# Performance work log

Hardware: AMD Instinct MI355X
Metric: run time of the kernel (lower is better)

The kernel has to match this reference:

```python
import jax, jax.numpy as jnp
import numpy as np

B, N, H, G, WIN, MH = 8, 8192, 128, 16, 3, 16
EPS = 1e-8


def _edges(n, w):
    # local sequence edges: i -> j for j in [i-w, i+w], j != i, 0 <= j < n
    i = np.arange(n)
    off = np.concatenate([np.arange(-w, 0), np.arange(1, w + 1)])
    j = i[:, None] + off[None, :]
    m = (j >= 0) & (j < n)
    src = np.broadcast_to(i[:, None], j.shape)[m]
    dst = j[m]
    return jnp.asarray(src, jnp.int32), jnp.asarray(dst, jnp.int32)


def setup_inputs() -> dict:
    key = jax.random.key(0)
    ks = jax.random.split(key, 10)
    d = {}
    d['x_scalar'] = jax.random.normal(ks[0], (B, N, H), jnp.float32)
    d['vec'] = jax.random.normal(ks[1], (B, N, 3, H), jnp.float32)
    d['W_geom'] = jax.random.normal(ks[2], (H, G), jnp.float32) / np.sqrt(H).astype(np.float32)
    d['q_w1'] = jax.random.normal(ks[3], (2, MH), jnp.float32) * 0.5
    d['q_b1'] = jnp.zeros((MH,), jnp.float32)
    d['q_w2'] = jax.random.normal(ks[4], (MH, 1), jnp.float32) * 0.25
    d['q_b2'] = jnp.zeros((1,), jnp.float32)
    d['k_w1'] = jax.random.normal(ks[5], (2, MH), jnp.float32) * 0.5
    d['k_b1'] = jnp.zeros((MH,), jnp.float32)
    d['k_w2'] = jax.random.normal(ks[6], (MH, 1), jnp.float32) * 0.25
    d['k_b2'] = jnp.zeros((1,), jnp.float32)
    d['Wq'] = jax.random.normal(ks[7], (G, H), jnp.float32) / np.sqrt(G).astype(np.float32)
    d['bq'] = jnp.zeros((H,), jnp.float32)
    d['Wk'] = jax.random.normal(ks[8], (G, H), jnp.float32) / np.sqrt(G).astype(np.float32)
    d['bk'] = jnp.zeros((H,), jnp.float32)
    return d


def _mlp(f, w1, b1, w2, b2):
    # f: (B,E,G,2) -> (B,E,G)
    return (jax.nn.silu(f @ w1 + b1) @ w2 + b2)[..., 0]


def reference(x_scalar, vec, W_geom, q_w1, q_b1, q_w2, q_b2,
              k_w1, k_b1, k_w2, k_b2, Wq, bq, Wk, bk):
    b, n, h = x_scalar.shape
    src, dst = _edges(n, WIN)
    # project vectors into geometry subspace: (B,N,3,G)
    vec_geom = jnp.einsum('bnch,hg->bncg', vec, W_geom)
    v_i = vec_geom[:, src]          # (B,E,3,G)
    v_j = vec_geom[:, dst]
    b_ij = v_j - v_i
    norm_b = jnp.maximum(jnp.linalg.norm(b_ij, axis=2, keepdims=True), EPS)
    e_ij = b_ij / norm_b            # unit edge directions (B,E,3,G)
    # scatter-add edge directions back to source nodes: (B,N,3,G)
    u = jnp.zeros((b, n, 3, G), x_scalar.dtype).at[:, src].add(e_ij)
    u_i = u[:, src]
    u_j = u[:, dst]
    dot_ui_e = (u_i * e_ij).sum(axis=2)                       # (B,E,G)
    norm_ui = jnp.maximum(jnp.linalg.norm(u_i, axis=2), EPS)
    ang_ij = jnp.clip(dot_ui_e / norm_ui, -1.0, 1.0)
    u_i_perp = u_i - dot_ui_e[:, :, None, :] * e_ij
    dot_uj_e = (u_j * e_ij).sum(axis=2)
    u_j_perp = u_j - dot_uj_e[:, :, None, :] * e_ij
    dot_perp = (u_i_perp * u_j_perp).sum(axis=2)
    np_i = jnp.maximum(jnp.linalg.norm(u_i_perp, axis=2), EPS)
    np_j = jnp.maximum(jnp.linalg.norm(u_j_perp, axis=2), EPS)
    dih_cos = jnp.clip(dot_perp / jnp.maximum(np_i * np_j, EPS), -1.0, 1.0)
    feats = jnp.stack([ang_ij, dih_cos], axis=-1)             # (B,E,G,2)
    g_geom_q = _mlp(feats, q_w1, q_b1, q_w2, q_b2)            # (B,E,G)
    g_geom_k = _mlp(feats, k_w1, k_b1, k_w2, k_b2)
    g_q = jax.nn.sigmoid(g_geom_q @ Wq + bq)                  # (B,E,H)
    g_k = jax.nn.sigmoid(g_geom_k @ Wk + bk)
    s_j = x_scalar[:, dst]                                    # (B,E,H)
    q = jnp.zeros_like(x_scalar).at[:, src].add(g_q * s_j)
    k = jnp.zeros_like(x_scalar).at[:, src].add(g_k * s_j)
    return q, k
```

## Files before the change

kernel.cpp:

```cpp
#include <hip/hip_runtime.h>

constexpr int NB = 8;
constexpr int NN = 8192;
constexpr int NH = 128;
constexpr int NG = 16;
constexpr float EPS = 1e-8f;
constexpr int NT = 48;
constexpr int NT1 = NT + 1;

typedef short s16x8 __attribute__((ext_vector_type(8)));
typedef float f32x4 __attribute__((ext_vector_type(4)));

__device__ __forceinline__ float frcp(float x) { return __builtin_amdgcn_rcpf(x); }
__device__ __forceinline__ float frsq(float x) { return __builtin_amdgcn_rsqf(x); }
__device__ __forceinline__ float fsigmoid(float x) { return frcp(1.f + __expf(-x)); }
__device__ __forceinline__ float fsilu(float x) { return x * fsigmoid(x); }
__device__ __forceinline__ float fclamp1(float x) { return fminf(fmaxf(x, -1.f), 1.f); }

__device__ __forceinline__ unsigned short f2bf(float x) {
    unsigned u = __builtin_bit_cast(unsigned, x);
    return (unsigned short)((u + 0x7FFFu + ((u >> 16) & 1u)) >> 16);
}
__device__ __forceinline__ unsigned packh2(float a, float b) {
    unsigned short lo = __builtin_bit_cast(unsigned short, (__fp16)a);
    unsigned short hi = __builtin_bit_cast(unsigned short, (__fp16)b);
    return (unsigned)lo | ((unsigned)hi << 16);
}
__device__ __forceinline__ float h2lo(unsigned u) {
    return (float)__builtin_bit_cast(__fp16, (unsigned short)(u & 0xFFFFu));
}
__device__ __forceinline__ float h2hi(unsigned u) {
    return (float)__builtin_bit_cast(__fp16, (unsigned short)(u >> 16));
}

__global__ __launch_bounds__(256) void k_table(
    const float* __restrict__ qw1, const float* __restrict__ qb1,
    const float* __restrict__ qw2, const float* __restrict__ qb2,
    const float* __restrict__ kw1, const float* __restrict__ kb1,
    const float* __restrict__ kw2, const float* __restrict__ kb2,
    unsigned* __restrict__ T) {
    int idx = blockIdx.x * 256 + threadIdx.x;
    if (idx >= NT1 * NT1) return;
    int ia = idx / NT1, id = idx % NT1;
    float a = -1.f + (float)ia * (2.f / NT);
    float d = -1.f + (float)id * (2.f / NT);
    float fq = qb2[0], fk = kb2[0];
#pragma unroll
    for (int m = 0; m < 16; ++m) {
        float hq = fmaf(a, qw1[m], fmaf(d, qw1[16 + m], qb1[m]));
        float hk = fmaf(a, kw1[m], fmaf(d, kw1[16 + m], kb1[m]));
        fq = fmaf(fsilu(hq), qw2[m], fq);
        fk = fmaf(fsilu(hk), kw2[m], fk);
    }
    T[idx] = packh2(fq, fk);
}

__global__ __launch_bounds__(256) void k_vecgeom(const float* __restrict__ vec,
                                                 const float* __restrict__ Wg,
                                                 float* __restrict__ vg) {
    __shared__ float Wl[NH * NG];
    for (int t = threadIdx.x; t < NH * NG; t += 256) Wl[t] = Wg[t];
    __syncthreads();

    int idx = blockIdx.x * 256 + threadIdx.x;
    int gq = idx & 3;
    int rc = idx >> 2;
    const float4* vrow = reinterpret_cast<const float4*>(vec + rc * NH);
    float a0 = 0.f, a1 = 0.f, a2 = 0.f, a3 = 0.f;
#pragma unroll 8
    for (int h4 = 0; h4 < 32; ++h4) {
        float4 v = vrow[h4];
        int h = h4 * 4;
        float4 w0 = *reinterpret_cast<const float4*>(&Wl[(h + 0) * NG + gq * 4]);
        float4 w1 = *reinterpret_cast<const float4*>(&Wl[(h + 1) * NG + gq * 4]);
        float4 w2 = *reinterpret_cast<const float4*>(&Wl[(h + 2) * NG + gq * 4]);
        float4 w3 = *reinterpret_cast<const float4*>(&Wl[(h + 3) * NG + gq * 4]);
        a0 = fmaf(v.x, w0.x, a0); a1 = fmaf(v.x, w0.y, a1); a2 = fmaf(v.x, w0.z, a2); a3 = fmaf(v.x, w0.w, a3);
        a0 = fmaf(v.y, w1.x, a0); a1 = fmaf(v.y, w1.y, a1); a2 = fmaf(v.y, w1.z, a2); a3 = fmaf(v.y, w1.w, a3);
        a0 = fmaf(v.z, w2.x, a0); a1 = fmaf(v.z, w2.y, a1); a2 = fmaf(v.z, w2.z, a2); a3 = fmaf(v.z, w2.w, a3);
        a0 = fmaf(v.w, w3.x, a0); a1 = fmaf(v.w, w3.y, a1); a2 = fmaf(v.w, w3.z, a2); a3 = fmaf(v.w, w3.w, a3);
    }
    *reinterpret_cast<float4*>(vg + rc * NG + gq * 4) = make_float4(a0, a1, a2, a3);
}

__global__ __launch_bounds__(256) void k_u(const float* __restrict__ vg,
                                           float* __restrict__ u) {
    int idx = blockIdx.x * 256 + threadIdx.x;
    int g = idx & 15;
    int bn = idx >> 4;
    int n = bn & (NN - 1);
    int base_i = bn * 48 + g;
    float vi0 = vg[base_i], vi1 = vg[base_i + 16], vi2 = vg[base_i + 32];
    float a0 = 0.f, a1 = 0.f, a2 = 0.f;
#pragma unroll
    for (int e = 0; e < 6; ++e) {
        int off = (e < 3) ? (e - 3) : (e - 2);
        int j = n + off;
        if (j < 0 || j >= NN) continue;
        int base_j = base_i + off * 48;
        float d0 = vg[base_j] - vi0;
        float d1 = vg[base_j + 16] - vi1;
        float d2 = vg[base_j + 32] - vi2;
        float r = frsq(fmaxf(d0 * d0 + d1 * d1 + d2 * d2, 1e-16f));
        a0 = fmaf(d0, r, a0); a1 = fmaf(d1, r, a1); a2 = fmaf(d2, r, a2);
    }
    u[base_i] = a0; u[base_i + 16] = a1; u[base_i + 32] = a2;
}

template <bool INT>
__device__ __forceinline__ void run_group(
    int bn0, int n0, int w, int lane,
    const float* __restrict__ vg, const float* __restrict__ u,
    const float* __restrict__ xs, const unsigned (&Ts)[NT1 * NT1],
    unsigned short (&As)[4][2][6][16][16], const s16x8 (&Wl)[2][8][64],
    const float (&bneg)[16],
    float* __restrict__ outq, float* __restrict__ outk) {

    int nl = lane >> 4, g = lane & 15;

#pragma unroll
    for (int nq = 0; nq < 4; ++nq) {
        int node = nq * 4 + nl;
        int bn = bn0 + node;
        int base_i = bn * 48 + g;
        float vi0 = vg[base_i], vi1 = vg[base_i + 16], vi2 = vg[base_i + 32];
        float ui0 = u[base_i],  ui1 = u[base_i + 16],  ui2 = u[base_i + 32];
        float rnui = frsq(fmaxf(ui0 * ui0 + ui1 * ui1 + ui2 * ui2, 1e-16f));
#pragma unroll
        for (int e = 0; e < 6; ++e) {
            int off = (e < 3) ? (e - 3) : (e - 2);
            bool valid = INT || ((unsigned)(n0 + node + off) < (unsigned)NN);
            float fq = 0.f, fk = 0.f;
            if (valid) {
                int base_j = base_i + off * 48;
                float d0 = vg[base_j] - vi0;
                float d1 = vg[base_j + 16] - vi1;
                float d2 = vg[base_j + 32] - vi2;
                float rb = frsq(fmaxf(d0 * d0 + d1 * d1 + d2 * d2, 1e-16f));
                float e0 = d0 * rb, e1 = d1 * rb, e2 = d2 * rb;
                float uj0 = u[base_j], uj1 = u[base_j + 16], uj2 = u[base_j + 32];
                float die = ui0 * e0 + ui1 * e1 + ui2 * e2;
                float ang = fclamp1(die * rnui);
                float p0 = ui0 - die * e0, p1 = ui1 - die * e1, p2 = ui2 - die * e2;
                float dje = uj0 * e0 + uj1 * e1 + uj2 * e2;
                float q0 = uj0 - dje * e0, q1 = uj1 - dje * e1, q2 = uj2 - dje * e2;
                float dp = p0 * q0 + p1 * q1 + p2 * q2;
                float pp = fmaxf(p0 * p0 + p1 * p1 + p2 * p2, 1e-16f);
                float qq = fmaxf(q0 * q0 + q1 * q1 + q2 * q2, 1e-16f);
                float dih = fclamp1(dp * frsq(pp * qq));

                float af = fmaf(ang, (float)NT * 0.5f, (float)NT * 0.5f);
                float df_ = fmaf(dih, (float)NT * 0.5f, (float)NT * 0.5f);
                int ia = min((int)af, NT - 1);
                int id = min((int)df_, NT - 1);
                float fa = af - (float)ia;
                float fd = df_ - (float)id;
                const unsigned* t0 = &Ts[ia * NT1 + id];
                unsigned c00 = t0[0], c01 = t0[1], c10 = t0[NT1], c11 = t0[NT1 + 1];
                float l0q = fmaf(fd, h2lo(c01) - h2lo(c00), h2lo(c00));
                float h0q = fmaf(fd, h2lo(c11) - h2lo(c10), h2lo(c10));
                fq = fmaf(fa, h0q - l0q, l0q);
                float l0k = fmaf(fd, h2hi(c01) - h2hi(c00), h2hi(c00));
                float h0k = fmaf(fd, h2hi(c11) - h2hi(c10), h2hi(c10));
                fk = fmaf(fa, h0k - l0k, l0k);
            }
            As[w][0][e][node][g] = f2bf(fq);
            As[w][1][e][node][g] = f2bf(fk);
        }
    }
    asm volatile("" ::: "memory");

    s16x8 afr[2][6];
    int aidx = (lane & 15) * 2 + (lane >> 4);
#pragma unroll
    for (int qk = 0; qk < 2; ++qk)
#pragma unroll
        for (int e = 0; e < 6; ++e)
            afr[qk][e] = (lane < 32)
                ? reinterpret_cast<const s16x8*>(&As[w][qk][e][0][0])[aidx]
                : (s16x8)0;

    const float* xw = xs + (bn0 + (lane >> 4) * 4) * NH + (lane & 15);
    float* oq = outq + (bn0 + (lane >> 4) * 4) * NH + (lane & 15);
    float* ok = outk + (bn0 + (lane >> 4) * 4) * NH + (lane & 15);
    f32x4 zero4 = {0.f, 0.f, 0.f, 0.f};

#pragma unroll
    for (int qk = 0; qk < 2; ++qk) {
#pragma unroll
        for (int ht = 0; ht < 8; ++ht) {
            s16x8 bfr = Wl[qk][ht][lane];
            f32x4 acc = zero4;
            float bn_ = bneg[qk * 8 + ht];
#pragma unroll
            for (int e = 0; e < 6; ++e) {
                f32x4 c = __builtin_amdgcn_mfma_f32_16x16x32_bf16(
                    afr[qk][e], bfr, zero4, 0, 0, 0);
                int off = (e < 3) ? (e - 3) : (e - 2);
                const float* xp = xw + off * NH + ht * 16;
#pragma unroll
                for (int r = 0; r < 4; ++r) {
                    float sneg = bn_ - c[r];
                    float p = frcp(1.f + __expf(sneg));
                    float xv;
                    if (INT) {
                        xv = xp[r * NH];
                    } else {
                        int jn = n0 + (lane >> 4) * 4 + r + off;
                        bool v2 = (unsigned)jn < (unsigned)NN;
                        const float* xq = v2 ? (xp + r * NH) : xs;
                        xv = *xq;
                        p = v2 ? p : 0.f;
                    }
                    acc[r] = fmaf(p, xv, acc[r]);
                }
            }
            float* o = (qk ? ok : oq) + ht * 16;
#pragma unroll
            for (int r = 0; r < 4; ++r) o[r * NH] = acc[r];
        }
    }
    asm volatile("" ::: "memory");
}

__global__ __launch_bounds__(256) void k_main(
    const float* __restrict__ vg, const float* __restrict__ u,
    const float* __restrict__ xs, const unsigned* __restrict__ T,
    const float* __restrict__ Wq, const float* __restrict__ bq,
    const float* __restrict__ Wk, const float* __restrict__ bk,
    float* __restrict__ outq, float* __restrict__ outk) {
    __shared__ unsigned Ts[NT1 * NT1];
    __shared__ unsigned short As[4][2][6][16][16];
    __shared__ s16x8 Wl[2][8][64];

    int tid = threadIdx.x;
    for (int t = tid; t < NT1 * NT1; t += 256) Ts[t] = T[t];

    for (int slot = tid; slot < 2 * 8 * 64; slot += 256) {
        int lane_in = slot & 63;
        int frag = slot >> 6;
        int fqk = frag >> 3, fht = frag & 7;
        s16x8 v = (s16x8)0;
        if (lane_in < 32) {
            const float* W = fqk ? Wk : Wq;
            int k0 = (lane_in >> 4) * 8, fcol = lane_in & 15;
#pragma unroll
            for (int i = 0; i < 8; ++i)
                v[i] = (short)f2bf(W[(k0 + i) * NH + fht * 16 + fcol]);
        }
        Wl[fqk][fht][lane_in] = v;
    }

    int w = tid >> 6, lane = tid & 63;
    int col = lane & 15;
    float bneg[16];
#pragma unroll
    for (int ht = 0; ht < 8; ++ht) {
        bneg[ht]     = -bq[ht * 16 + col];
        bneg[8 + ht] = -bk[ht * 16 + col];
    }
    __syncthreads();

    int grp = blockIdx.x * 4 + w;
    int bn0 = grp * 16;
    int n0 = bn0 & (NN - 1);
    bool interior = (n0 != 0) && (n0 != NN - 16);
    if (interior)
        run_group<true>(bn0, n0, w, lane, vg, u, xs, Ts, As, Wl, bneg, outq, outk);
    else
        run_group<false>(bn0, n0, w, lane, vg, u, xs, Ts, As, Wl, bneg, outq, outk);
}

extern "C" void kernel_launch(void* const* d_in, const int* in_sizes, int n_in,
                              void* d_out, int out_size, void* d_ws, size_t ws_size,
                              hipStream_t stream) {
    const float* xs   = (const float*)d_in[0];
    const float* vec  = (const float*)d_in[1];
    const float* Wg   = (const float*)d_in[2];
    const float* qw1  = (const float*)d_in[3];
    const float* qb1  = (const float*)d_in[4];
    const float* qw2  = (const float*)d_in[5];
    const float* qb2  = (const float*)d_in[6];
    const float* kw1  = (const float*)d_in[7];
    const float* kb1  = (const float*)d_in[8];
    const float* kw2  = (const float*)d_in[9];
    const float* kb2  = (const float*)d_in[10];
    const float* Wq   = (const float*)d_in[11];
    const float* bq   = (const float*)d_in[12];
    const float* Wk   = (const float*)d_in[13];
    const float* bk   = (const float*)d_in[14];

    float* vg = (float*)d_ws;
    float* u  = vg + (size_t)NB * NN * 3 * NG;
    unsigned* T = (unsigned*)(u + (size_t)NB * NN * 3 * NG);
    float* outq = (float*)d_out;
    float* outk = outq + (size_t)NB * NN * NH;

    k_table<<<dim3((NT1 * NT1 + 255) / 256), dim3(256), 0, stream>>>(
        qw1, qb1, qw2, qb2, kw1, kb1, kw2, kb2, T);
    k_vecgeom<<<dim3(3072), dim3(256), 0, stream>>>(vec, Wg, vg);
    k_u<<<dim3(4096), dim3(256), 0, stream>>>(vg, u);
    k_main<<<dim3(1024), dim3(256), 0, stream>>>(
        vg, u, xs, T, Wq, bq, Wk, bk, outq, outk);
}
```

Measured before the change: 94.22 us.

## Permute output columns so each lane reuses x rows across edges and stores float2

The output column mapping is permuted so each lane owns 8 interleaved columns. The 10 x_scalar rows a lane needs are loaded once as float2 and reused across all six edges and both q and k, instead of reloading a scalar per edge. Stores become float2, biases move to shared memory, the W fragment table is halved, and launch bounds request 4 blocks per SM. NT also changes from 48 to 36, which alters the lookup table size in code not shown. Register pressure from the xr buffer and the two accumulators could hurt occupancy.

```diff
diff --git a/kernel.cpp b/kernel.cpp
--- a/kernel.cpp
+++ b/kernel.cpp
@@ -4,8 +4,7 @@
 constexpr int NN = 8192;
 constexpr int NH = 128;
 constexpr int NG = 16;
-constexpr float EPS = 1e-8f;
-constexpr int NT = 48;
+constexpr int NT = 36;
 constexpr int NT1 = NT + 1;
 
 typedef short s16x8 __attribute__((ext_vector_type(8)));
@@ -112,8 +111,8 @@
     int bn0, int n0, int w, int lane,
     const float* __restrict__ vg, const float* __restrict__ u,
     const float* __restrict__ xs, const unsigned (&Ts)[NT1 * NT1],
-    unsigned short (&As)[4][2][6][16][16], const s16x8 (&Wl)[2][8][64],
-    const float (&bneg)[16],
+    unsigned short (&As)[4][2][6][16][16], const s16x8 (&Wl)[2][8][32],
+    const float (&bs)[2][NH],
     float* __restrict__ outq, float* __restrict__ outk) {
 
     int nl = lane >> 4, g = lane & 15;
@@ -180,85 +179,90 @@
                 ? reinterpret_cast<const s16x8*>(&As[w][qk][e][0][0])[aidx]
                 : (s16x8)0;
 
-    const float* xw = xs + (bn0 + (lane >> 4) * 4) * NH + (lane & 15);
-    float* oq = outq + (bn0 + (lane >> 4) * 4) * NH + (lane & 15);
-    float* ok = outk + (bn0 + (lane >> 4) * 4) * NH + (lane & 15);
+    int c = lane & 15;
+    int rg = lane >> 4;
+    const float* xbase = xs + (bn0 + rg * 4) * NH + c * 8;
     f32x4 zero4 = {0.f, 0.f, 0.f, 0.f};
 
 #pragma unroll
-    for (int qk = 0; qk < 2; ++qk) {
-#pragma unroll
-        for (int ht = 0; ht < 8; ++ht) {
-            s16x8 bfr = Wl[qk][ht][lane];
-            f32x4 acc = zero4;
-            float bn_ = bneg[qk * 8 + ht];
+    for (int p4 = 0; p4 < 4; ++p4) {
+        float2 xr[10];
+#pragma unroll
+        for (int d = 0; d < 10; ++d) {
+            if (INT) {
+                xr[d] = *reinterpret_cast<const float2*>(xbase + (d - 3) * NH + p4 * 2);
+            } else {
+                int gidx = bn0 + rg * 4 + d - 3;
+                gidx = min(max(gidx, 0), NB * NN - 1);
+                xr[d] = *reinterpret_cast<const float2*>(xs + (size_t)gidx * NH + c * 8 + p4 * 2);
+            }
+        }
+#pragma unroll
+        for (int qk = 0; qk < 2; ++qk) {
+            s16x8 bfr0 = (lane < 32) ? Wl[qk][2 * p4][lane] : (s16x8)0;
+            s16x8 bfr1 = (lane < 32) ? Wl[qk][2 * p4 + 1][lane] : (s16x8)0;
+            float b0 = bs[qk][c * 8 + 2 * p4];
+            float b1 = bs[qk][c * 8 + 2 * p4 + 1];
+            f32x4 a0 = zero4, a1 = zero4;
 #pragma unroll
             for (int e = 0; e < 6; ++e) {
-                f32x4 c = __builtin_amdgcn_mfma_f32_16x16x32_bf16(
-                    afr[qk][e], bfr, zero4, 0, 0, 0);
+                f32x4 c0 = __builtin_amdgcn_mfma_f32_16x16x32_bf16(afr[qk][e], bfr0, zero4, 0, 0, 0);
+                f32x4 c1 = __builtin_amdgcn_mfma_f32_16x16x32_bf16(afr[qk][e], bfr1, zero4, 0, 0, 0);
                 int off = (e < 3) ? (e - 3) : (e - 2);
-                const float* xp = xw + off * NH + ht * 16;
 #pragma unroll
                 for (int r = 0; r < 4; ++r) {
-                    float sneg = bn_ - c[r];
-                    float p = frcp(1.f + __expf(sneg));
-                    float xv;
-                    if (INT) {
-                        xv = xp[r * NH];
-                    } else {
-                        int jn = n0 + (lane >> 4) * 4 + r + off;
+                    float pr0 = fsigmoid(c0[r] + b0);
+                    float pr1 = fsigmoid(c1[r] + b1);
+                    if (!INT) {
+                        int jn = n0 + rg * 4 + r + off;
                         bool v2 = (unsigned)jn < (unsigned)NN;
-                        const float* xq = v2 ? (xp + r * NH) : xs;
-                        xv = *xq;
-                        p = v2 ? p : 0.f;
+                        pr0 = v2 ? pr0 : 0.f;
+                        pr1 = v2 ? pr1 : 0.f;
                     }
-                    acc[r] = fmaf(p, xv, acc[r]);
+                    float2 x2 = xr[r + off + 3];
+                    a0[r] = fmaf(pr0, x2.x, a0[r]);
+                    a1[r] = fmaf(pr1, x2.y, a1[r]);
                 }
             }
-            float* o = (qk ? ok : oq) + ht * 16;
-#pragma unroll
-            for (int r = 0; r < 4; ++r) o[r * NH] = acc[r];
+            float* o = (qk ? outk : outq) + (bn0 + rg * 4) * NH + c * 8 + p4 * 2;
+#pragma unroll
+            for (int r = 0; r < 4; ++r)
+                *reinterpret_cast<float2*>(o + r * NH) = make_float2(a0[r], a1[r]);
         }
     }
     asm volatile("" ::: "memory");
 }
 
-__global__ __launch_bounds__(256) void k_main(
+__global__ __launch_bounds__(256, 4) void k_main(
     const float* __restrict__ vg, const float* __restrict__ u,
     const float* __restrict__ xs, const unsigned* __restrict__ T,
     const float* __restrict__ Wq, const float* __restrict__ bq,
     const float* __restrict__ Wk, const float* __restrict__ bk,
     float* __restrict__ outq, float* __restrict__ outk) {
     __shared__ unsigned Ts[NT1 * NT1];
-    __shared__ unsigned short As[4][2][6][16][16];
-    __shared__ s16x8 Wl[2][8][64];
+    __shared__ __align__(16) unsigned short As[4][2][6][16][16];
+    __shared__ s16x8 Wl[2][8][32];
+    __shared__ float bs[2][NH];
 
     int tid = threadIdx.x;
     for (int t = tid; t < NT1 * NT1; t += 256) Ts[t] = T[t];
 
-    for (int slot = tid; slot < 2 * 8 * 64; slot += 256) {
-        int lane_in = slot & 63;
-        int frag = slot >> 6;
-        int fqk = frag >> 3, fht = frag & 7;
-        s16x8 v = (s16x8)0;
-        if (lane_in < 32) {
-            const float* W = fqk ? Wk : Wq;
-            int k0 = (lane_in >> 4) * 8, fcol = lane_in & 15;
-#pragma unroll
-            for (int i = 0; i < 8; ++i)
-                v[i] = (short)f2bf(W[(k0 + i) * NH + fht * 16 + fcol]);
-        }
-        Wl[fqk][fht][lane_in] = v;
-    }
+    for (int slot = tid; slot < 2 * 8 * 32; slot += 256) {
+        int lane_in = slot & 31;
+        int frag = slot >> 5;
+        int fqk = frag >> 3, t = frag & 7;
+        const float* W = fqk ? Wk : Wq;
+        int k0 = (lane_in >> 4) * 8, cc = lane_in & 15;
+        s16x8 v;
+#pragma unroll
+        for (int i = 0; i < 8; ++i)
+            v[i] = (short)f2bf(W[(k0 + i) * NH + cc * 8 + t]);
+        Wl[fqk][t][lane_in] = v;
+    }
+    if (tid < NH) bs[0][tid] = bq[tid];
+    else bs[1][tid - NH] = bk[tid - NH];
 
     int w = tid >> 6, lane = tid & 63;
-    int col = lane & 15;
-    float bneg[16];
-#pragma unroll
-    for (int ht = 0; ht < 8; ++ht) {
-        bneg[ht]     = -bq[ht * 16 + col];
-        bneg[8 + ht] = -bk[ht * 16 + col];
-    }
     __syncthreads();
 
     int grp = blockIdx.x * 4 + w;
@@ -266,9 +270,9 @@
     int n0 = bn0 & (NN - 1);
     bool interior = (n0 != 0) && (n0 != NN - 16);
     if (interior)
-        run_group<true>(bn0, n0, w, lane, vg, u, xs, Ts, As, Wl, bneg, outq, outk);
+        run_group<true>(bn0, n0, w, lane, vg, u, xs, Ts, As, Wl, bs, outq, outk);
     else
-        run_group<false>(bn0, n0, w, lane, vg, u, xs, Ts, As, Wl, bneg, outq, outk);
+        run_group<false>(bn0, n0, w, lane, vg, u, xs, Ts, As, Wl, bs, outq, outk);
 }
 
 extern "C" void kernel_launch(void* const* d_in, const int* in_sizes, int n_in,
```

Measured after the change: 139.0 us. +47.5%, slower.
